# Kernel tuning notes

Hardware: AMD Instinct MI355X
Metric: run time of the kernel (lower is better)

Reference implementation:

```python
import jax, jax.numpy as jnp
import numpy as np

B, T, C, H = 32, 1024, 384, 64

def setup_inputs() -> dict:
    key = jax.random.key(0)
    k1, k2, k3, k4 = jax.random.split(key, 4)
    x = jax.random.normal(k1, (B, T, C), dtype=jnp.float32)
    s = 1.0 / np.sqrt(C)
    Wk = jax.random.normal(k2, (C, H), dtype=jnp.float32) * s
    Wq = jax.random.normal(k3, (C, H), dtype=jnp.float32) * s
    Wv = jax.random.normal(k4, (C, H), dtype=jnp.float32) * s
    return {"x": x, "Wk": Wk, "Wq": Wq, "Wv": Wv}

def reference(x, Wk, Wq, Wv):
    # Single-head causal attention (dropout = identity, eval mode).
    Tn = x.shape[1]
    k = jnp.einsum('btc,ch->bth', x, Wk)   # [B,T,H]
    q = jnp.einsum('btc,ch->bth', x, Wq)
    v = jnp.einsum('btc,ch->bth', x, Wv)
    scale = k.shape[-1] ** -0.5
    wei = jnp.einsum('bth,bsh->bts', q, k) * scale  # [B,T,T]
    causal = jnp.tril(jnp.ones((Tn, Tn), dtype=bool))
    wei = jnp.where(causal, wei, -jnp.inf)
    wei = jax.nn.softmax(wei, axis=-1)
    out = jnp.einsum('bts,bsh->bth', wei, v)  # [B,T,H]
    return out
```

## Files before the change

### kernel.cpp

```cpp
#include <hip/hip_runtime.h>

#define BB 32
#define TT 1024
#define CCH 384
#define HH 64

typedef short short8 __attribute__((ext_vector_type(8)));
typedef float f32x4 __attribute__((ext_vector_type(4)));
typedef unsigned short ushort;

static __device__ __forceinline__ ushort f2bf(float f) {
    union { float f; unsigned u; } v; v.f = f;
    unsigned r = v.u + 0x7fff + ((v.u >> 16) & 1);
    return (ushort)(r >> 16);
}

__global__ void wswz(const float* __restrict__ Wk, const float* __restrict__ Wq,
                     const float* __restrict__ Wv, ushort* __restrict__ wf) {
    const int mat = blockIdx.x, ks = blockIdx.y;
    const float* W = (mat == 0) ? Wk : ((mat == 1) ? Wq : Wv);
    const int t = threadIdx.x;
    const int ct = t >> 6, lane = t & 63, quad = lane >> 4, l15 = lane & 15;
    const int col = ct * 16 + l15;
    short8 d;
#pragma unroll
    for (int j = 0; j < 8; ++j)
        d[j] = (short)f2bf(W[(ks * 32 + quad * 8 + j) * 64 + col]);
    *(short8*)(wf + (((mat * 12 + ks) * 4 + ct) << 9) + lane * 8) = d;
}

#define XSTR 388
#define VS_STRIDE 68

__global__ __launch_bounds__(256, 2) void qkv(const float* __restrict__ x,
                                              const ushort* __restrict__ wf,
                                              ushort* __restrict__ kb,
                                              ushort* __restrict__ qb,
                                              ushort* __restrict__ vtb) {
    const int r0 = blockIdx.x * 64;
    const int tid = threadIdx.x;
    const int wv = tid >> 6, lane = tid & 63, l15 = lane & 15, quad = lane >> 4;

    __shared__ ushort xs[64 * XSTR];

#pragma unroll
    for (int kb3 = 0; kb3 < 3; ++kb3) {
        const int kbase = kb3 * 128;
        const int seg = (tid & 7) * 16;
#pragma unroll
        for (int i = 0; i < 2; ++i) {
            const int r = (tid >> 3) + 32 * i;
            const float* src = x + (size_t)(r0 + r) * CCH + kbase + seg;
            f32x4 v0 = *(const f32x4*)(src);
            f32x4 v1 = *(const f32x4*)(src + 4);
            f32x4 v2 = *(const f32x4*)(src + 8);
            f32x4 v3 = *(const f32x4*)(src + 12);
            short8 p0, p1;
#pragma unroll
            for (int j = 0; j < 4; ++j) {
                p0[j]     = (short)f2bf(v0[j]);
                p0[j + 4] = (short)f2bf(v1[j]);
                p1[j]     = (short)f2bf(v2[j]);
                p1[j + 4] = (short)f2bf(v3[j]);
            }
            *(short8*)(xs + r * XSTR + kbase + seg) = p0;
            *(short8*)(xs + r * XSTR + kbase + seg + 8) = p1;
        }
    }
    __syncthreads();

    f32x4 acc[12] = {};
    short8 bf[2][12];
#pragma unroll
    for (int m = 0; m < 3; ++m)
#pragma unroll
        for (int ct = 0; ct < 4; ++ct)
            bf[0][m * 4 + ct] = *(const short8*)(wf + (((m * 12 + 0) * 4 + ct) << 9) + lane * 8);

#pragma unroll
    for (int ks = 0; ks < 12; ++ks) {
        short8 a = *(const short8*)(xs + (wv * 16 + l15) * XSTR + ks * 32 + quad * 8);
        if (ks < 11) {
#pragma unroll
            for (int m = 0; m < 3; ++m)
#pragma unroll
                for (int ct = 0; ct < 4; ++ct)
                    bf[(ks + 1) & 1][m * 4 + ct] =
                        *(const short8*)(wf + (((m * 12 + ks + 1) * 4 + ct) << 9) + lane * 8);
        }
#pragma unroll
        for (int f = 0; f < 12; ++f)
            acc[f] = __builtin_amdgcn_mfma_f32_16x16x32_bf16(a, bf[ks & 1][f], acc[f], 0, 0, 0);
    }

#pragma unroll
    for (int ct = 0; ct < 4; ++ct) {
#pragma unroll
        for (int r = 0; r < 4; ++r) {
            int row = r0 + wv * 16 + quad * 4 + r;
            int col = ct * 16 + l15;
            kb[row * 64 + col] = f2bf(acc[0 + ct][r]);
            qb[row * 64 + col] = f2bf(acc[4 + ct][r]);
        }
    }
    __syncthreads();
    ushort* vs = xs;
#pragma unroll
    for (int ct = 0; ct < 4; ++ct)
#pragma unroll
        for (int r = 0; r < 4; ++r)
            vs[(wv * 16 + quad * 4 + r) * VS_STRIDE + ct * 16 + l15] = f2bf(acc[8 + ct][r]);
    __syncthreads();
    {
        const int col = tid >> 2;
        const int rbase = (tid & 3) * 16;
        short8 d0, d1;
#pragma unroll
        for (int j = 0; j < 8; ++j) {
            d0[j] = (short)vs[(rbase + j) * VS_STRIDE + col];
            d1[j] = (short)vs[(rbase + 8 + j) * VS_STRIDE + col];
        }
        const int b = r0 >> 10;
        const int t = (r0 & 1023) + rbase;
        *(short8*)(vtb + b * 65536 + col * 1024 + t) = d0;
        *(short8*)(vtb + b * 65536 + col * 1024 + t + 8) = d1;
    }
}

#define PSTR 136

__global__ __launch_bounds__(256, 2) void attn(const ushort* __restrict__ qb,
                                               const ushort* __restrict__ kb,
                                               const ushort* __restrict__ vtb,
                                               float* __restrict__ out) {
    const int y = blockIdx.y;
    const int qt = (y < 8) ? (15 - y) : (y - 8);
    const int b = blockIdx.x;
    const int t0 = qt * 64;
    const int tid = threadIdx.x;
    const int wv = tid >> 6, lane = tid & 63, l15 = lane & 15, quad = lane >> 4;

    __shared__ ushort Ks[128 * 72];
    __shared__ ushort Vs[64 * 136];
    __shared__ ushort Ps[4 * 16 * PSTR];
    ushort* Psw = Ps + wv * 16 * PSTR;

    const int qrow = b * 1024 + t0 + wv * 16 + l15;
    short8 qf0 = *(const short8*)(qb + qrow * 64 + quad * 8);
    short8 qf1 = *(const short8*)(qb + qrow * 64 + 32 + quad * 8);

    f32x4 o[4] = {};
    float li[4] = {0.f, 0.f, 0.f, 0.f};
    const float c1 = 0.125f * 1.4426950408889634f;
    const float c2 = 10.0f * 1.4426950408889634f;

    const int nst = (qt >> 1) + 1;

    short8 kr[4], vr[4];
#pragma unroll
    for (int i = 0; i < 4; ++i) {
        int c = tid + i * 256;
        kr[i] = *(const short8*)(kb + (b * 1024 + (c >> 3)) * 64 + (c & 7) * 8);
        vr[i] = *(const short8*)(vtb + b * 65536 + (c >> 4) * 1024 + (c & 15) * 8);
    }

    for (int it = 0; it < nst; ++it) {
        const int s0 = it * 128;
        __syncthreads();
#pragma unroll
        for (int i = 0; i < 4; ++i) {
            int c = tid + i * 256;
            *(short8*)(Ks + (c >> 3) * 72 + (c & 7) * 8) = kr[i];
            *(short8*)(Vs + (c >> 4) * 136 + (c & 15) * 8) = vr[i];
        }
        __syncthreads();
        if (it + 1 < nst) {
            const int sn = s0 + 128;
#pragma unroll
            for (int i = 0; i < 4; ++i) {
                int c = tid + i * 256;
                kr[i] = *(const short8*)(kb + (b * 1024 + sn + (c >> 3)) * 64 + (c & 7) * 8);
                vr[i] = *(const short8*)(vtb + b * 65536 + (c >> 4) * 1024 + sn + (c & 15) * 8);
            }
        }

        f32x4 s[8];
        __builtin_amdgcn_s_setprio(1);
#pragma unroll
        for (int ct = 0; ct < 8; ++ct) {
            f32x4 z = {};
            short8 b0 = *(const short8*)(Ks + (ct * 16 + l15) * 72 + quad * 8);
            z = __builtin_amdgcn_mfma_f32_16x16x32_bf16(qf0, b0, z, 0, 0, 0);
            short8 b1 = *(const short8*)(Ks + (ct * 16 + l15) * 72 + 32 + quad * 8);
            s[ct] = __builtin_amdgcn_mfma_f32_16x16x32_bf16(qf1, b1, z, 0, 0, 0);
        }
        __builtin_amdgcn_s_setprio(0);

        if (it + 1 < nst) {
#pragma unroll
            for (int r = 0; r < 4; ++r) {
#pragma unroll
                for (int ct = 0; ct < 8; ++ct) {
                    float p = exp2f(s[ct][r] * c1 - c2);
                    li[r] += p;
                    Psw[(quad * 4 + r) * PSTR + ct * 16 + l15] = f2bf(p);
                }
            }
        } else {
#pragma unroll
            for (int r = 0; r < 4; ++r) {
                const int trow = t0 + wv * 16 + quad * 4 + r;
#pragma unroll
                for (int ct = 0; ct < 8; ++ct) {
                    int col = s0 + ct * 16 + l15;
                    float p = (col <= trow) ? exp2f(s[ct][r] * c1 - c2) : 0.f;
                    li[r] += p;
                    Psw[(quad * 4 + r) * PSTR + ct * 16 + l15] = f2bf(p);
                }
            }
        }

        short8 pa[4];
#pragma unroll
        for (int kk = 0; kk < 4; ++kk)
            pa[kk] = *(const short8*)(Psw + l15 * PSTR + kk * 32 + quad * 8);

        __builtin_amdgcn_s_setprio(1);
#pragma unroll
        for (int ct = 0; ct < 4; ++ct) {
#pragma unroll
            for (int kk = 0; kk < 4; ++kk) {
                short8 vb = *(const short8*)(Vs + (ct * 16 + l15) * 136 + kk * 32 + quad * 8);
                o[ct] = __builtin_amdgcn_mfma_f32_16x16x32_bf16(pa[kk], vb, o[ct], 0, 0, 0);
            }
        }
        __builtin_amdgcn_s_setprio(0);
    }

#pragma unroll
    for (int r = 0; r < 4; ++r) {
        float rs = li[r];
#pragma unroll
        for (int off = 1; off < 16; off <<= 1)
            rs += __shfl_xor(rs, off);
        float inv = 1.0f / rs;
        int t = t0 + wv * 16 + quad * 4 + r;
#pragma unroll
        for (int ct = 0; ct < 4; ++ct) {
            int h = ct * 16 + l15;
            out[b * 65536 + t * 64 + h] = o[ct][r] * inv;
        }
    }
}

extern "C" void kernel_launch(void* const* d_in, const int* in_sizes, int n_in,
                              void* d_out, int out_size, void* d_ws, size_t ws_size,
                              hipStream_t stream) {
    const float* x  = (const float*)d_in[0];
    const float* Wk = (const float*)d_in[1];
    const float* Wq = (const float*)d_in[2];
    const float* Wv = (const float*)d_in[3];

    char* ws = (char*)d_ws;
    ushort* wf  = (ushort*)ws;
    ushort* kb  = (ushort*)(ws + 256 * 1024);
    ushort* qb  = (ushort*)(ws + 256 * 1024 + 4u * 1024 * 1024);
    ushort* vtb = (ushort*)(ws + 256 * 1024 + 8u * 1024 * 1024);

    wswz<<<dim3(3, 12), dim3(256), 0, stream>>>(Wk, Wq, Wv, wf);
    qkv<<<dim3(512), dim3(256), 0, stream>>>(x, wf, kb, qb, vtb);
    attn<<<dim3(32, 16), dim3(256), 0, stream>>>(qb, kb, vtb, (float*)d_out);
}
```

Baseline: 122.2 us.

## Double-buffer K in LDS and load V fragments directly from global

Stops staging V^T in shared memory. Each wave now loads its V MFMA operands straight from global memory into registers at the start of each step. K moves to a double-buffered LDS array with the next tile's register prefetch, which cuts the per-iteration barriers from two to one. This lowers LDS footprint and synchronisation, but every wave now issues redundant global loads for V (each of the 4 waves reads the whole V tile), and the 16 short8 V registers add register pressure.

```diff
diff --git a/kernel.cpp b/kernel.cpp
--- a/kernel.cpp
+++ b/kernel.cpp
@@ -128,6 +128,7 @@
 }
 
 #define PSTR 136
+#define KSTR 72
 
 __global__ __launch_bounds__(256, 2) void attn(const ushort* __restrict__ qb,
                                                const ushort* __restrict__ kb,
@@ -140,10 +141,12 @@
     const int tid = threadIdx.x;
     const int wv = tid >> 6, lane = tid & 63, l15 = lane & 15, quad = lane >> 4;
 
-    __shared__ ushort Ks[128 * 72];
-    __shared__ ushort Vs[64 * 136];
+    __shared__ ushort Ks[2][128 * KSTR];
     __shared__ ushort Ps[4 * 16 * PSTR];
     ushort* Psw = Ps + wv * 16 * PSTR;
+
+    const ushort* kbb = kb  + (size_t)b * 65536;
+    const ushort* vbb = vtb + (size_t)b * 65536;
 
     const int qrow = b * 1024 + t0 + wv * 16 + l15;
     short8 qf0 = *(const short8*)(qb + qrow * 64 + quad * 8);
@@ -156,31 +159,50 @@
 
     const int nst = (qt >> 1) + 1;
 
-    short8 kr[4], vr[4];
+    short8 kr[4];
 #pragma unroll
     for (int i = 0; i < 4; ++i) {
         int c = tid + i * 256;
-        kr[i] = *(const short8*)(kb + (b * 1024 + (c >> 3)) * 64 + (c & 7) * 8);
-        vr[i] = *(const short8*)(vtb + b * 65536 + (c >> 4) * 1024 + (c & 15) * 8);
-    }
+        kr[i] = *(const short8*)(kbb + (c >> 3) * 64 + (c & 7) * 8);
+    }
+#pragma unroll
+    for (int i = 0; i < 4; ++i) {
+        int c = tid + i * 256;
+        *(short8*)(Ks[0] + (c >> 3) * KSTR + (c & 7) * 8) = kr[i];
+    }
+    if (nst > 1) {
+#pragma unroll
+        for (int i = 0; i < 4; ++i) {
+            int c = tid + i * 256;
+            kr[i] = *(const short8*)(kbb + (128 + (c >> 3)) * 64 + (c & 7) * 8);
+        }
+    }
+    __syncthreads();
 
     for (int it = 0; it < nst; ++it) {
         const int s0 = it * 128;
-        __syncthreads();
-#pragma unroll
-        for (int i = 0; i < 4; ++i) {
-            int c = tid + i * 256;
-            *(short8*)(Ks + (c >> 3) * 72 + (c & 7) * 8) = kr[i];
-            *(short8*)(Vs + (c >> 4) * 136 + (c & 15) * 8) = vr[i];
-        }
-        __syncthreads();
+        const ushort* Kc = Ks[it & 1];
+
+        short8 vb[4][4];
+#pragma unroll
+        for (int ct = 0; ct < 4; ++ct)
+#pragma unroll
+            for (int kk = 0; kk < 4; ++kk)
+                vb[ct][kk] = *(const short8*)(vbb + (ct * 16 + l15) * 1024 + s0 + kk * 32 + quad * 8);
+
         if (it + 1 < nst) {
-            const int sn = s0 + 128;
+            ushort* Kn = Ks[(it + 1) & 1];
 #pragma unroll
             for (int i = 0; i < 4; ++i) {
                 int c = tid + i * 256;
-                kr[i] = *(const short8*)(kb + (b * 1024 + sn + (c >> 3)) * 64 + (c & 7) * 8);
-                vr[i] = *(const short8*)(vtb + b * 65536 + (c >> 4) * 1024 + sn + (c & 15) * 8);
+                *(short8*)(Kn + (c >> 3) * KSTR + (c & 7) * 8) = kr[i];
+            }
+            if (it + 2 < nst) {
+#pragma unroll
+                for (int i = 0; i < 4; ++i) {
+                    int c = tid + i * 256;
+                    kr[i] = *(const short8*)(kbb + ((it + 2) * 128 + (c >> 3)) * 64 + (c & 7) * 8);
+                }
             }
         }
 
@@ -189,9 +211,9 @@
 #pragma unroll
         for (int ct = 0; ct < 8; ++ct) {
             f32x4 z = {};
-            short8 b0 = *(const short8*)(Ks + (ct * 16 + l15) * 72 + quad * 8);
+            short8 b0 = *(const short8*)(Kc + (ct * 16 + l15) * KSTR + quad * 8);
             z = __builtin_amdgcn_mfma_f32_16x16x32_bf16(qf0, b0, z, 0, 0, 0);
-            short8 b1 = *(const short8*)(Ks + (ct * 16 + l15) * 72 + 32 + quad * 8);
+            short8 b1 = *(const short8*)(Kc + (ct * 16 + l15) * KSTR + 32 + quad * 8);
             s[ct] = __builtin_amdgcn_mfma_f32_16x16x32_bf16(qf1, b1, z, 0, 0, 0);
         }
         __builtin_amdgcn_s_setprio(0);
@@ -229,12 +251,12 @@
 #pragma unroll
         for (int ct = 0; ct < 4; ++ct) {
 #pragma unroll
-            for (int kk = 0; kk < 4; ++kk) {
-                short8 vb = *(const short8*)(Vs + (ct * 16 + l15) * 136 + kk * 32 + quad * 8);
-                o[ct] = __builtin_amdgcn_mfma_f32_16x16x32_bf16(pa[kk], vb, o[ct], 0, 0, 0);
-            }
+            for (int kk = 0; kk < 4; ++kk)
+                o[ct] = __builtin_amdgcn_mfma_f32_16x16x32_bf16(pa[kk], vb[ct][kk], o[ct], 0, 0, 0);
         }
         __builtin_amdgcn_s_setprio(0);
+
+        __syncthreads();
     }
 
 #pragma unroll
```

Measured after the change: 129.3 us. 1.06x slower.
